# Optimization experiments

Measured on AMD Instinct MI355X. Metric: run time of the kernel, lower is better.

Reference implementation:

```python
import jax, jax.numpy as jnp
import numpy as np

B, N, D, K, DSPACE, NFREQ = 4, 4096, 256, 16, 3, 5
BN_EPS = 1e-5


def setup_inputs() -> dict:
    key = jax.random.key(0)
    ks = jax.random.split(key, 12)
    s = 1.0 / np.sqrt(D)
    pe_in = DSPACE * 2 * NFREQ + DSPACE  # 33
    return {
        "xyz": jax.random.normal(ks[0], (B, N, DSPACE), jnp.float32),
        "feats": jax.random.normal(ks[1], (B, N, D), jnp.float32),
        "w_q": jax.random.uniform(ks[2], (D, D), jnp.float32, -s, s),
        "w_k": jax.random.uniform(ks[3], (D, D), jnp.float32, -s, s),
        "w_v": jax.random.uniform(ks[4], (D, D), jnp.float32, -s, s),
        "g_w1": jax.random.uniform(ks[5], (D, D), jnp.float32, -s, s),
        "g_b1": jax.random.uniform(ks[6], (D,), jnp.float32, -s, s),
        "g_w2": jax.random.uniform(ks[7], (D, D), jnp.float32, -s, s),
        "g_b2": jax.random.uniform(ks[8], (D,), jnp.float32, -s, s),
        "pe_w": jax.random.uniform(ks[9], (D, pe_in), jnp.float32, -s, s),
        "pe_b": jax.random.uniform(ks[10], (D,), jnp.float32, -s, s),
        "bn_w": jnp.ones((D,), jnp.float32),
        "bn_b": jnp.zeros((D,), jnp.float32),
    }


def _gather_knn(points, idx):
    # points [b,n,c], idx [b,n,k] -> [b,n,k,c]
    return jax.vmap(lambda p, i: p[i])(points, idx)


def reference(xyz, feats, w_q, w_k, w_v, g_w1, g_b1, g_w2, g_b2, pe_w, pe_b, bn_w, bn_b):
    # KNN (no grad in original): full pairwise sq-distance + top-k smallest
    dists = jnp.sum((xyz[:, :, None] - xyz[:, None]) ** 2, axis=-1)  # [b,n,n]
    _, knn_idx = jax.lax.top_k(-dists, K)  # [b,n,k], ascending distance
    knn_idx = jax.lax.stop_gradient(knn_idx)
    knn_xyz = jax.lax.stop_gradient(_gather_knn(xyz, knn_idx))  # [b,n,k,3]

    q = feats @ w_q.T                               # [b,n,d]
    k_g = _gather_knn(feats @ w_k.T, knn_idx)       # [b,n,k,d]
    v_g = _gather_knn(feats @ w_v.T, knn_idx)       # [b,n,k,d]

    pos_diff = xyz[:, :, None] - knn_xyz            # [b,n,k,3]
    freqs = jnp.linspace(1.0, 2.0 ** NFREQ, NFREQ).astype(pos_diff.dtype)
    embeds = [pos_diff]
    for f in freqs:
        embeds.append(jnp.sin(pos_diff * f))
        embeds.append(jnp.cos(pos_diff * f))
    pos_embed = jnp.concatenate(embeds, axis=-1)    # [b,n,k,33]
    pos_encode = pos_embed @ pe_w.T + pe_b          # [b,n,k,d]

    edges = q[:, :, None] - k_g + pos_encode        # [b,n,k,d]
    h = jax.nn.relu(edges @ g_w1.T + g_b1)
    attn = h @ g_w2.T + g_b2                        # [b,n,k,d]
    attn = jax.nn.softmax(attn, axis=-2)            # softmax over neighbors

    res = jnp.einsum('bnkf,bnkf->bnf', attn, v_g + pos_encode) + feats

    # BatchNorm1d over channel dim, training-mode batch stats (biased var)
    mean = jnp.mean(res, axis=(0, 1))
    var = jnp.var(res, axis=(0, 1))
    res = (res - mean) * jax.lax.rsqrt(var + BN_EPS) * bn_w + bn_b
    return res
```

## Files before the change

### kernel.cpp

```cpp
#include <hip/hip_runtime.h>

#define BB 4
#define NN 4096
#define DD 256
#define KK 16
#define PTS 2

typedef __bf16 bf16;
typedef __attribute__((ext_vector_type(8))) __bf16 bf16x8;
typedef __attribute__((ext_vector_type(4))) __bf16 bf16x4;
typedef __attribute__((ext_vector_type(4))) float f32x4;

__global__ __launch_bounds__(256) void prep_kernel(
    const float* __restrict__ wq, const float* __restrict__ wk,
    const float* __restrict__ wv, const float* __restrict__ w1,
    const float* __restrict__ w2, const float* __restrict__ pw,
    bf16* __restrict__ wqb, bf16* __restrict__ wkb, bf16* __restrict__ wvb,
    bf16* __restrict__ w1b, bf16* __restrict__ w2b, bf16* __restrict__ pwb) {
  const int idx = blockIdx.x * 256 + threadIdx.x;
  wqb[idx] = (bf16)wq[idx];
  wkb[idx] = (bf16)wk[idx];
  wvb[idx] = (bf16)wv[idx];
  w1b[idx] = (bf16)w1[idx];
  w2b[idx] = (bf16)w2[idx];
  if (idx < 256 * 64) {
    const int n = idx >> 6, c = idx & 63;
    pwb[idx] = (c < 33) ? (bf16)pw[n * 33 + c] : (bf16)0.f;
  }
}

__global__ __launch_bounds__(256, 2) void knn_v2(const float* __restrict__ xyz,
                                                 int* __restrict__ knn) {
  const int lane = threadIdx.x & 63;
  const int wv = threadIdx.x >> 6;
  const int row = blockIdx.x * 4 + wv;
  const int b = row >> 12, i = row & (NN - 1);
  const float* xb = xyz + (size_t)b * NN * 3;
  const float xi = xb[i * 3 + 0], yi = xb[i * 3 + 1], zi = xb[i * 3 + 2];
  unsigned long long cand[64];
#pragma unroll
  for (int c = 0; c < 64; ++c) {
    const int j = c * 64 + lane;
    const float dx = xi - xb[j * 3 + 0];
    const float dy = yi - xb[j * 3 + 1];
    const float dz = zi - xb[j * 3 + 2];
    const float d = dx * dx + dy * dy + dz * dz;
    const unsigned long long fb = (unsigned long long)(__float_as_uint(d)) + 1ull;
    cand[c] = (fb << 32) | (unsigned int)j;
  }
  unsigned long long lastkey = 0ull;
  unsigned int myj = 0u;
  for (int r = 0; r < KK; ++r) {
    unsigned long long lmin = ~0ull;
#pragma unroll
    for (int c = 0; c < 64; ++c) {
      const unsigned long long v = cand[c];
      if (v > lastkey && v < lmin) lmin = v;
    }
#pragma unroll
    for (int off = 1; off < 64; off <<= 1) {
      const unsigned long long o = __shfl_xor(lmin, off);
      if (o < lmin) lmin = o;
    }
    if (lane == r) myj = (unsigned int)lmin;
    lastkey = lmin;
  }
  if (lane < KK) knn[row * KK + lane] = (int)myj;
}

__global__ __launch_bounds__(256, 4) void proj_mfma(
    const float* __restrict__ feats, const bf16* __restrict__ wqb,
    const bf16* __restrict__ wkb, const bf16* __restrict__ wvb,
    float* __restrict__ q, bf16* __restrict__ kfb, bf16* __restrict__ vfb) {
  const int t = threadIdx.x;
  const int lane = t & 63, wv = t >> 6;
  const int m = lane & 15, qd = lane >> 4;
  const size_t r0 = (size_t)blockIdx.x * 64;
  __shared__ __align__(16) bf16 fs[64][264];
  const float4* f4 = (const float4*)(feats + r0 * DD);
  for (int i = 0; i < 16; ++i) {
    const int e = i * 256 + t;
    const float4 v = f4[e];
    bf16x4 w;
    w[0] = (bf16)v.x; w[1] = (bf16)v.y; w[2] = (bf16)v.z; w[3] = (bf16)v.w;
    *(bf16x4*)&fs[e >> 6][(e & 63) * 4] = w;
  }
  __syncthreads();
  bf16x8 afrag[8];
#pragma unroll
  for (int f = 0; f < 8; ++f)
    afrag[f] = *(const bf16x8*)&fs[wv * 16 + m][f * 32 + qd * 8];
  const bf16* wmat[3] = {wqb, wkb, wvb};
  for (int mat = 0; mat < 3; ++mat) {
    const bf16* wb = wmat[mat];
    for (int nt = 0; nt < 16; ++nt) {
      const int n = nt * 16 + m;
      bf16x8 bfr[8];
#pragma unroll
      for (int f = 0; f < 8; ++f)
        bfr[f] = *(const bf16x8*)(wb + (size_t)n * DD + f * 32 + qd * 8);
      f32x4 c = {0.f, 0.f, 0.f, 0.f};
#pragma unroll
      for (int f = 0; f < 8; ++f)
        c = __builtin_amdgcn_mfma_f32_16x16x32_bf16(afrag[f], bfr[f], c, 0, 0, 0);
#pragma unroll
      for (int rr = 0; rr < 4; ++rr) {
        const size_t o = (r0 + wv * 16 + qd * 4 + rr) * DD + n;
        if (mat == 0) q[o] = c[rr];
        else if (mat == 1) kfb[o] = (bf16)c[rr];
        else vfb[o] = (bf16)c[rr];
      }
    }
  }
}

__global__ __launch_bounds__(256, 3) void edge_v3(
    const float* __restrict__ xyz, const float* __restrict__ feats,
    const float* __restrict__ q, const bf16* __restrict__ kfb,
    const bf16* __restrict__ vfb, const int* __restrict__ knn,
    const bf16* __restrict__ w1b, const float* __restrict__ g_b1,
    const bf16* __restrict__ w2b, const float* __restrict__ g_b2,
    const bf16* __restrict__ pwb, const float* __restrict__ pe_b,
    float* __restrict__ res) {
  const int t = threadIdx.x;
  const int lane = t & 63;
  const int wv = t >> 6;
  const int m = lane & 15;
  const int qd = lane >> 4;
  const int row0 = blockIdx.x * PTS;
  const int b = row0 >> 12;

  __shared__ __align__(16) bf16 emb_s[PTS][16][88];
  __shared__ __align__(16) bf16 bufA[PTS][16][264];
  __shared__ __align__(16) bf16 bufB[PTS][16][264];
  __shared__ int js_s[PTS][16];

  if (t < PTS * 16) js_s[t >> 4][t & 15] = knn[(row0 + (t >> 4)) * KK + (t & 15)];
  __syncthreads();

  const float* xb = xyz + (size_t)b * NN * 3;
  for (int p = 0; p < PTS; ++p) {
    const int i = (row0 + p) & (NN - 1);
    for (int e = t; e < 16 * 88; e += 256) {
      const int k = e / 88, c = e % 88;
      float val = 0.f;
      if (c < 33) {
        const int cc = (c < 3) ? c : (c - 3) % 3;
        const float pd = xb[i * 3 + cc] - xb[js_s[p][k] * 3 + cc];
        if (c < 3) {
          val = pd;
        } else {
          const int f = (c - 3) / 6;
          const float x = pd * fmaf(7.75f, (float)f, 1.0f);
          val = (((c - 3) % 6) < 3) ? __sinf(x) : __cosf(x);
        }
      }
      emb_s[p][k][c] = (bf16)val;
    }
  }
  __syncthreads();

  float vpe[4][PTS][4];
#pragma unroll
  for (int tt = 0; tt < 4; ++tt) {
    const int n = wv * 64 + tt * 16 + m;
    const bf16x8 b0 = *(const bf16x8*)(pwb + (size_t)n * 64 + qd * 8);
    const bf16x8 b1 = *(const bf16x8*)(pwb + (size_t)n * 64 + 32 + qd * 8);
    const float bias = pe_b[n];
#pragma unroll
    for (int p = 0; p < PTS; ++p) {
      const bf16x8 a0 = *(const bf16x8*)&emb_s[p][m][qd * 8];
      const bf16x8 a1 = *(const bf16x8*)&emb_s[p][m][32 + qd * 8];
      f32x4 c = {bias, bias, bias, bias};
      c = __builtin_amdgcn_mfma_f32_16x16x32_bf16(a0, b0, c, 0, 0, 0);
      c = __builtin_amdgcn_mfma_f32_16x16x32_bf16(a1, b1, c, 0, 0, 0);
      const float qv = q[(size_t)(row0 + p) * DD + n];
#pragma unroll
      for (int rr = 0; rr < 4; ++rr) {
        const int krow = qd * 4 + rr;
        const size_t jr = ((size_t)(b * NN + js_s[p][krow])) * DD + n;
        bufA[p][krow][n] = (bf16)(qv - (float)kfb[jr] + c[rr]);
        vpe[tt][p][rr] = (float)vfb[jr] + c[rr];
      }
    }
  }
  __syncthreads();

  {
    bf16x8 afrag[PTS][8];
#pragma unroll
    for (int p = 0; p < PTS; ++p)
#pragma unroll
      for (int f = 0; f < 8; ++f)
        afrag[p][f] = *(const bf16x8*)&bufA[p][m][f * 32 + qd * 8];
    for (int tt = 0; tt < 4; ++tt) {
      const int n = wv * 64 + tt * 16 + m;
      bf16x8 bfr[8];
#pragma unroll
      for (int f = 0; f < 8; ++f)
        bfr[f] = *(const bf16x8*)(w1b + (size_t)n * DD + f * 32 + qd * 8);
      const float bias = g_b1[n];
#pragma unroll
      for (int p = 0; p < PTS; ++p) {
        f32x4 c = {bias, bias, bias, bias};
#pragma unroll
        for (int f = 0; f < 8; ++f)
          c = __builtin_amdgcn_mfma_f32_16x16x32_bf16(afrag[p][f], bfr[f], c, 0, 0, 0);
#pragma unroll
        for (int rr = 0; rr < 4; ++rr)
          bufB[p][qd * 4 + rr][n] = (bf16)fmaxf(c[rr], 0.f);
      }
    }
  }
  __syncthreads();

  {
    bf16x8 afrag[PTS][8];
#pragma unroll
    for (int p = 0; p < PTS; ++p)
#pragma unroll
      for (int f = 0; f < 8; ++f)
        afrag[p][f] = *(const bf16x8*)&bufB[p][m][f * 32 + qd * 8];
#pragma unroll
    for (int tt = 0; tt < 4; ++tt) {
      const int n = wv * 64 + tt * 16 + m;
      bf16x8 bfr[8];
#pragma unroll
      for (int f = 0; f < 8; ++f)
        bfr[f] = *(const bf16x8*)(w2b + (size_t)n * DD + f * 32 + qd * 8);
      const float bias = g_b2[n];
#pragma unroll
      for (int p = 0; p < PTS; ++p) {
        f32x4 c = {bias, bias, bias, bias};
#pragma unroll
        for (int f = 0; f < 8; ++f)
          c = __builtin_amdgcn_mfma_f32_16x16x32_bf16(afrag[p][f], bfr[f], c, 0, 0, 0);
        float mx = fmaxf(fmaxf(c[0], c[1]), fmaxf(c[2], c[3]));
        mx = fmaxf(mx, __shfl_xor(mx, 16));
        mx = fmaxf(mx, __shfl_xor(mx, 32));
        float e[4], den = 0.f;
#pragma unroll
        for (int rr = 0; rr < 4; ++rr) {
          e[rr] = __expf(c[rr] - mx);
          den += e[rr];
        }
        den += __shfl_xor(den, 16);
        den += __shfl_xor(den, 32);
        float num = 0.f;
#pragma unroll
        for (int rr = 0; rr < 4; ++rr) num += e[rr] * vpe[tt][p][rr];
        num += __shfl_xor(num, 16);
        num += __shfl_xor(num, 32);
        if (qd == 0) {
          const size_t o = (size_t)(row0 + p) * DD + n;
          res[o] = num / den + feats[o];
        }
      }
    }
  }
}

__global__ __launch_bounds__(256) void bn_stats(const float* __restrict__ res,
                                                float* __restrict__ sums,
                                                float* __restrict__ sumsq) {
  const int t = threadIdx.x;
  const size_t r0 = (size_t)blockIdx.x * 32;
  float s = 0.f, s2 = 0.f;
  for (int r = 0; r < 32; ++r) {
    const float v = res[(r0 + r) * DD + t];
    s += v;
    s2 += v * v;
  }
  atomicAdd(&sums[t], s);
  atomicAdd(&sumsq[t], s2);
}

__global__ __launch_bounds__(256) void bn_apply(float* __restrict__ out,
                                                const float* __restrict__ sums,
                                                const float* __restrict__ sumsq,
                                                const float* __restrict__ bn_w,
                                                const float* __restrict__ bn_b) {
  const int idx = blockIdx.x * 256 + threadIdx.x;
  const int c = idx & (DD - 1);
  const float inv_n = 1.f / (float)(BB * NN);
  const float mean = sums[c] * inv_n;
  const float var = sumsq[c] * inv_n - mean * mean;
  const float v = out[idx];
  out[idx] = (v - mean) * rsqrtf(var + 1e-5f) * bn_w[c] + bn_b[c];
}

extern "C" void kernel_launch(void* const* d_in, const int* in_sizes, int n_in,
                              void* d_out, int out_size, void* d_ws,
                              size_t ws_size, hipStream_t stream) {
  (void)in_sizes; (void)n_in; (void)out_size; (void)ws_size;
  const float* xyz = (const float*)d_in[0];
  const float* feats = (const float*)d_in[1];
  const float* w_q = (const float*)d_in[2];
  const float* w_k = (const float*)d_in[3];
  const float* w_v = (const float*)d_in[4];
  const float* g_w1 = (const float*)d_in[5];
  const float* g_b1 = (const float*)d_in[6];
  const float* g_w2 = (const float*)d_in[7];
  const float* g_b2 = (const float*)d_in[8];
  const float* pe_w = (const float*)d_in[9];
  const float* pe_b = (const float*)d_in[10];
  const float* bn_w = (const float*)d_in[11];
  const float* bn_b = (const float*)d_in[12];
  float* out = (float*)d_out;

  const int BN = BB * NN;
  char* w = (char*)d_ws;
  int* knn = (int*)w;       w += (size_t)BN * KK * 4;
  float* q = (float*)w;     w += (size_t)BN * DD * 4;
  bf16* kfb = (bf16*)w;     w += (size_t)BN * DD * 2;
  bf16* vfb = (bf16*)w;     w += (size_t)BN * DD * 2;
  float* sums = (float*)w;  w += DD * 4;
  float* sumsq = (float*)w; w += DD * 4;
  bf16* wqb = (bf16*)w;     w += (size_t)DD * DD * 2;
  bf16* wkb = (bf16*)w;     w += (size_t)DD * DD * 2;
  bf16* wvb = (bf16*)w;     w += (size_t)DD * DD * 2;
  bf16* w1b = (bf16*)w;     w += (size_t)DD * DD * 2;
  bf16* w2b = (bf16*)w;     w += (size_t)DD * DD * 2;
  bf16* pwb = (bf16*)w;     w += (size_t)DD * 64 * 2;

  prep_kernel<<<DD * DD / 256, 256, 0, stream>>>(w_q, w_k, w_v, g_w1, g_w2,
                                                 pe_w, wqb, wkb, wvb, w1b, w2b,
                                                 pwb);
  knn_v2<<<BN / 4, 256, 0, stream>>>(xyz, knn);
  proj_mfma<<<BN / 64, 256, 0, stream>>>(feats, wqb, wkb, wvb, q, kfb, vfb);
  edge_v3<<<BN / PTS, 256, 0, stream>>>(xyz, feats, q, kfb, vfb, knn, w1b, g_b1,
                                        w2b, g_b2, pwb, pe_b, out);
  hipMemsetAsync(sums, 0, 2 * DD * sizeof(float), stream);
  bn_stats<<<BN / 32, 256, 0, stream>>>(out, sums, sumsq);
  bn_apply<<<BN, 256, 0, stream>>>(out, sums, sumsq, bn_w, bn_b);
}
```

Before: 679.5 us.

## Rework KNN selection, shrink projection tiles, pad and alias edge LDS buffers

```diff
diff --git a/kernel.cpp b/kernel.cpp
--- a/kernel.cpp
+++ b/kernel.cpp
@@ -5,6 +5,8 @@
 #define DD 256
 #define KK 16
 #define PTS 2
+#define SA 280
+#define SE 104
 
 typedef __bf16 bf16;
 typedef __attribute__((ext_vector_type(8))) __bf16 bf16x8;
@@ -16,7 +18,8 @@
     const float* __restrict__ wv, const float* __restrict__ w1,
     const float* __restrict__ w2, const float* __restrict__ pw,
     bf16* __restrict__ wqb, bf16* __restrict__ wkb, bf16* __restrict__ wvb,
-    bf16* __restrict__ w1b, bf16* __restrict__ w2b, bf16* __restrict__ pwb) {
+    bf16* __restrict__ w1b, bf16* __restrict__ w2b, bf16* __restrict__ pwb,
+    float* __restrict__ sums) {
   const int idx = blockIdx.x * 256 + threadIdx.x;
   wqb[idx] = (bf16)wq[idx];
   wkb[idx] = (bf16)wk[idx];
@@ -27,9 +30,10 @@
     const int n = idx >> 6, c = idx & 63;
     pwb[idx] = (c < 33) ? (bf16)pw[n * 33 + c] : (bf16)0.f;
   }
-}
-
-__global__ __launch_bounds__(256, 2) void knn_v2(const float* __restrict__ xyz,
+  if (idx < 2 * DD) sums[idx] = 0.f;
+}
+
+__global__ __launch_bounds__(256, 2) void knn_v3(const float* __restrict__ xyz,
                                                  int* __restrict__ knn) {
   const int lane = threadIdx.x & 63;
   const int wv = threadIdx.x >> 6;
@@ -48,22 +52,39 @@
     const unsigned long long fb = (unsigned long long)(__float_as_uint(d)) + 1ull;
     cand[c] = (fb << 32) | (unsigned int)j;
   }
-  unsigned long long lastkey = 0ull;
+  unsigned long long gm[8];
+#pragma unroll
+  for (int g = 0; g < 8; ++g) {
+    unsigned long long mn = cand[g * 8];
+#pragma unroll
+    for (int s = 1; s < 8; ++s)
+      if (cand[g * 8 + s] < mn) mn = cand[g * 8 + s];
+    gm[g] = mn;
+  }
   unsigned int myj = 0u;
   for (int r = 0; r < KK; ++r) {
-    unsigned long long lmin = ~0ull;
-#pragma unroll
-    for (int c = 0; c < 64; ++c) {
-      const unsigned long long v = cand[c];
-      if (v > lastkey && v < lmin) lmin = v;
-    }
+    unsigned long long lmin = gm[0];
+#pragma unroll
+    for (int g = 1; g < 8; ++g)
+      if (gm[g] < lmin) lmin = gm[g];
 #pragma unroll
     for (int off = 1; off < 64; off <<= 1) {
       const unsigned long long o = __shfl_xor(lmin, off);
       if (o < lmin) lmin = o;
     }
     if (lane == r) myj = (unsigned int)lmin;
-    lastkey = lmin;
+#pragma unroll
+    for (int g = 0; g < 8; ++g) {
+      if (__ballot(gm[g] == lmin)) {
+        unsigned long long nm = ~0ull;
+#pragma unroll
+        for (int s = 0; s < 8; ++s) {
+          const unsigned long long v = cand[g * 8 + s];
+          if (v > lmin && v < nm) nm = v;
+        }
+        if (gm[g] == lmin) gm[g] = nm;
+      }
+    }
   }
   if (lane < KK) knn[row * KK + lane] = (int)myj;
 }
@@ -75,10 +96,11 @@
   const int t = threadIdx.x;
   const int lane = t & 63, wv = t >> 6;
   const int m = lane & 15, qd = lane >> 4;
-  const size_t r0 = (size_t)blockIdx.x * 64;
-  __shared__ __align__(16) bf16 fs[64][264];
+  const size_t r0 = (size_t)blockIdx.x * 16;
+  __shared__ __align__(16) bf16 fs[16][SA];
   const float4* f4 = (const float4*)(feats + r0 * DD);
-  for (int i = 0; i < 16; ++i) {
+#pragma unroll
+  for (int i = 0; i < 4; ++i) {
     const int e = i * 256 + t;
     const float4 v = f4[e];
     bf16x4 w;
@@ -89,12 +111,12 @@
   bf16x8 afrag[8];
 #pragma unroll
   for (int f = 0; f < 8; ++f)
-    afrag[f] = *(const bf16x8*)&fs[wv * 16 + m][f * 32 + qd * 8];
+    afrag[f] = *(const bf16x8*)&fs[m][f * 32 + qd * 8];
   const bf16* wmat[3] = {wqb, wkb, wvb};
   for (int mat = 0; mat < 3; ++mat) {
     const bf16* wb = wmat[mat];
-    for (int nt = 0; nt < 16; ++nt) {
-      const int n = nt * 16 + m;
+    for (int nt = 0; nt < 4; ++nt) {
+      const int n = wv * 64 + nt * 16 + m;
       bf16x8 bfr[8];
 #pragma unroll
       for (int f = 0; f < 8; ++f)
@@ -105,7 +127,7 @@
         c = __builtin_amdgcn_mfma_f32_16x16x32_bf16(afrag[f], bfr[f], c, 0, 0, 0);
 #pragma unroll
       for (int rr = 0; rr < 4; ++rr) {
-        const size_t o = (r0 + wv * 16 + qd * 4 + rr) * DD + n;
+        const size_t o = (r0 + qd * 4 + rr) * DD + n;
         if (mat == 0) q[o] = c[rr];
         else if (mat == 1) kfb[o] = (bf16)c[rr];
         else vfb[o] = (bf16)c[rr];
@@ -114,7 +136,7 @@
   }
 }
 
-__global__ __launch_bounds__(256, 3) void edge_v3(
+__global__ __launch_bounds__(256, 4) void edge_v5(
     const float* __restrict__ xyz, const float* __restrict__ feats,
     const float* __restrict__ q, const bf16* __restrict__ kfb,
     const bf16* __restrict__ vfb, const int* __restrict__ knn,
@@ -130,37 +152,51 @@
   const int row0 = blockIdx.x * PTS;
   const int b = row0 >> 12;
 
-  __shared__ __align__(16) bf16 emb_s[PTS][16][88];
-  __shared__ __align__(16) bf16 bufA[PTS][16][264];
-  __shared__ __align__(16) bf16 bufB[PTS][16][264];
+  __shared__ __align__(16) bf16 bufA[PTS][16][SA];
+  __shared__ __align__(16) char un_s[PTS * 16 * SA * 2];
+  bf16(*bufB)[16][SA] = (bf16(*)[16][SA])un_s;
+  bf16(*emb_s)[16][SE] = (bf16(*)[16][SE])un_s;
   __shared__ int js_s[PTS][16];
 
   if (t < PTS * 16) js_s[t >> 4][t & 15] = knn[(row0 + (t >> 4)) * KK + (t & 15)];
   __syncthreads();
 
   const float* xb = xyz + (size_t)b * NN * 3;
+  {
+    const int k = t >> 4;
+    const int c0 = (t & 15) * 6;
+#pragma unroll
+    for (int p = 0; p < PTS; ++p) {
+      const int i = (row0 + p) & (NN - 1);
+      const int j = js_s[p][k];
+#pragma unroll
+      for (int cc = 0; cc < 6; ++cc) {
+        const int c = c0 + cc;
+        float val = 0.f;
+        if (c < 33) {
+          const int ax = (c < 3) ? c : (c - 3) % 3;
+          const float pd = xb[i * 3 + ax] - xb[j * 3 + ax];
+          if (c < 3) {
+            val = pd;
+          } else {
+            const int f = (c - 3) / 6;
+            const float x = pd * fmaf(7.75f, (float)f, 1.0f);
+            val = (((c - 3) % 6) < 3) ? __sinf(x) : __cosf(x);
+          }
+        }
+        emb_s[p][k][c] = (bf16)val;
+      }
+    }
+  }
+  __syncthreads();
+
+  float vpe[4][PTS][4];
+  bf16x8 ea0[PTS], ea1[PTS];
+#pragma unroll
   for (int p = 0; p < PTS; ++p) {
-    const int i = (row0 + p) & (NN - 1);
-    for (int e = t; e < 16 * 88; e += 256) {
-      const int k = e / 88, c = e % 88;
-      float val = 0.f;
-      if (c < 33) {
-        const int cc = (c < 3) ? c : (c - 3) % 3;
-        const float pd = xb[i * 3 + cc] - xb[js_s[p][k] * 3 + cc];
-        if (c < 3) {
-          val = pd;
-        } else {
-          const int f = (c - 3) / 6;
-          const float x = pd * fmaf(7.75f, (float)f, 1.0f);
-          val = (((c - 3) % 6) < 3) ? __sinf(x) : __cosf(x);
-        }
-      }
-      emb_s[p][k][c] = (bf16)val;
-    }
-  }
-  __syncthreads();
-
-  float vpe[4][PTS][4];
+    ea0[p] = *(const bf16x8*)&emb_s[p][m][qd * 8];
+    ea1[p] = *(const bf16x8*)&emb_s[p][m][32 + qd * 8];
+  }
 #pragma unroll
   for (int tt = 0; tt < 4; ++tt) {
     const int n = wv * 64 + tt * 16 + m;
@@ -169,11 +205,9 @@
     const float bias = pe_b[n];
 #pragma unroll
     for (int p = 0; p < PTS; ++p) {
-      const bf16x8 a0 = *(const bf16x8*)&emb_s[p][m][qd * 8];
-      const bf16x8 a1 = *(const bf16x8*)&emb_s[p][m][32 + qd * 8];
       f32x4 c = {bias, bias, bias, bias};
-      c = __builtin_amdgcn_mfma_f32_16x16x32_bf16(a0, b0, c, 0, 0, 0);
-      c = __builtin_amdgcn_mfma_f32_16x16x32_bf16(a1, b1, c, 0, 0, 0);
+      c = __builtin_amdgcn_mfma_f32_16x16x32_bf16(ea0[p], b0, c, 0, 0, 0);
+      c = __builtin_amdgcn_mfma_f32_16x16x32_bf16(ea1[p], b1, c, 0, 0, 0);
       const float qv = q[(size_t)(row0 + p) * DD + n];
 #pragma unroll
       for (int rr = 0; rr < 4; ++rr) {
@@ -325,12 +359,11 @@
 
   prep_kernel<<<DD * DD / 256, 256, 0, stream>>>(w_q, w_k, w_v, g_w1, g_w2,
                                                  pe_w, wqb, wkb, wvb, w1b, w2b,
-                                                 pwb);
-  knn_v2<<<BN / 4, 256, 0, stream>>>(xyz, knn);
-  proj_mfma<<<BN / 64, 256, 0, stream>>>(feats, wqb, wkb, wvb, q, kfb, vfb);
-  edge_v3<<<BN / PTS, 256, 0, stream>>>(xyz, feats, q, kfb, vfb, knn, w1b, g_b1,
+                                                 pwb, sums);
+  knn_v3<<<BN / 4, 256, 0, stream>>>(xyz, knn);
+  proj_mfma<<<BN / 16, 256, 0, stream>>>(feats, wqb, wkb, wvb, q, kfb, vfb);
+  edge_v5<<<BN / PTS, 256, 0, stream>>>(xyz, feats, q, kfb, vfb, knn, w1b, g_b1,
                                         w2b, g_b2, pwb, pe_b, out);
-  hipMemsetAsync(sums, 0, 2 * DD * sizeof(float), stream);
   bn_stats<<<BN / 32, 256, 0, stream>>>(out, sums, sumsq);
   bn_apply<<<BN, 256, 0, stream>>>(out, sums, sumsq, bn_w, bn_b);
 }
```

After: 694.8 us. +2.2%, slower.
